# Kernel tuning notes

Hardware: AMD Instinct MI355X
Metric: run time of the kernel (lower is better)

Reference implementation:

```python
import jax, jax.numpy as jnp
import numpy as np

V_SIZE = 128000  # vocab size (v_size init arg)


def setup_inputs() -> dict:
    key = jax.random.key(0)
    k1, k2 = jax.random.split(key)
    # per-position scores -> weighting_scheme (softmax over seq dim)
    w_es = jax.random.normal(k1, (256, 2048), dtype=jnp.float32)
    # instance['x']: token ids in [0, v_size)
    x = jax.random.randint(k2, (256, 2048), 0, V_SIZE, dtype=jnp.int64)
    return {"w_es": w_es, "x": x}


def reference(w_es, x):
    # weighting_scheme(indices, w_es, instance): softmax over sequence positions
    weights = jax.nn.softmax(w_es, axis=-1)          # [B, S]
    B, S = weights.shape
    rows = jnp.arange(B)[:, None]                    # [B, 1] broadcast against [B, S]
    # scatter: w_a[b, x[b, i]] = weights[b, i]  (vectorized index_put)
    w_a = jnp.zeros((B, V_SIZE), dtype=weights.dtype).at[rows, x].set(weights)
    return (w_a, weights)
```

## Files before the change

### kernel.cpp

```cpp
#include <hip/hip_runtime.h>

#define BATCH 256
#define SEQ   2048
#define VOCAB 128000
#define HALF  64000
#define HSLOT 4096

typedef float v4f __attribute__((ext_vector_type(4)));
typedef int   v4i __attribute__((ext_vector_type(4)));
typedef float v2f __attribute__((ext_vector_type(2)));
typedef int   v2i __attribute__((ext_vector_type(2)));

#define LBAR() do { asm volatile("s_waitcnt lgkmcnt(0)" ::: "memory"); \
                    __builtin_amdgcn_s_barrier(); } while (0)

__device__ __forceinline__ int hash_v(int v) {
    return (int)(((unsigned)v * 2654435761u) >> 20);
}

__global__ __launch_bounds__(1024, 4)
void softmax_zero_then_scatter(const float* __restrict__ w_es,
                               const int*   __restrict__ x,
                               float* __restrict__ w_a,
                               float* __restrict__ w_out)
{
    __shared__ int   key[HSLOT];
    __shared__ int   val[HSLOT];
    __shared__ float red[32];

    const int bid = blockIdx.x;
    const int r = bid & (BATCH - 1);
    const int h = bid >> 8;
    const int t = threadIdx.x;
    const int lane = t & 63;
    const int wid  = t >> 6;

    const v2f a  = ((const v2f*)(w_es + (size_t)r * SEQ))[t];
    const v2i xv = ((const v2i*)(x    + (size_t)r * SEQ))[t];

    ((v4i*)key)[t] = (v4i)(-1);
    ((v4i*)val)[t] = (v4i)(-1);

    __syncthreads();

    v4f* gp4 = (v4f*)(w_a + (size_t)r * VOCAB + h * HALF);
    {
        const v4f z = (v4f)(0.0f);
        #pragma unroll
        for (int j = 0; j < 15; ++j)
            gp4[j * 1024 + t] = z;
        if (t < 640)
            gp4[15 * 1024 + t] = z;
    }

    float m = fmaxf(a.x, a.y);
    #pragma unroll
    for (int off = 32; off > 0; off >>= 1)
        m = fmaxf(m, __shfl_down(m, off, 64));
    if (lane == 0) red[wid] = m;
    LBAR();
    m = red[0];
    #pragma unroll
    for (int k = 1; k < 16; ++k) m = fmaxf(m, red[k]);

    const float e0 = __expf(a.x - m);
    const float e1 = __expf(a.y - m);
    float s = e0 + e1;
    #pragma unroll
    for (int off = 32; off > 0; off >>= 1)
        s += __shfl_down(s, off, 64);
    if (lane == 0) red[16 + wid] = s;
    LBAR();
    s = red[16];
    #pragma unroll
    for (int k = 1; k < 16; ++k) s += red[16 + k];

    const float inv = 1.0f / s;
    const float w0 = e0 * inv;
    const float w1 = e1 * inv;

    if (h == 0) {
        v2f wv; wv.x = w0; wv.y = w1;
        ((v2f*)(w_out + (size_t)r * SEQ))[t] = wv;
    }

    const int i0 = 2 * t;
    const int i1 = 2 * t + 1;
    const int v0 = xv.x - h * HALF;
    const int v1 = xv.y - h * HALF;
    const bool in0 = (unsigned)v0 < (unsigned)HALF;
    const bool in1 = (unsigned)v1 < (unsigned)HALF;

    if (in0) {
        int sl = hash_v(v0);
        while (true) {
            int k = atomicCAS(&key[sl], -1, v0);
            if (k == -1 || k == v0) break;
            sl = (sl + 1) & (HSLOT - 1);
        }
        atomicMax(&val[sl], i0);
    }
    if (in1) {
        int sl = hash_v(v1);
        while (true) {
            int k = atomicCAS(&key[sl], -1, v1);
            if (k == -1 || k == v1) break;
            sl = (sl + 1) & (HSLOT - 1);
        }
        atomicMax(&val[sl], i1);
    }

    __syncthreads();

    float* gp = w_a + (size_t)r * VOCAB + h * HALF;
    if (in0) {
        int sl = hash_v(v0);
        while (key[sl] != v0) sl = (sl + 1) & (HSLOT - 1);
        if (val[sl] == i0) gp[v0] = w0;
    }
    if (in1) {
        int sl = hash_v(v1);
        while (key[sl] != v1) sl = (sl + 1) & (HSLOT - 1);
        if (val[sl] == i1) gp[v1] = w1;
    }
}

extern "C" void kernel_launch(void* const* d_in, const int* in_sizes, int n_in,
                              void* d_out, int out_size, void* d_ws, size_t ws_size,
                              hipStream_t stream) {
    const float* w_es = (const float*)d_in[0];
    const int*   x    = (const int*)d_in[1];

    float* out  = (float*)d_out;
    float* w_a  = out;
    float* w    = out + (size_t)BATCH * VOCAB;

    softmax_zero_then_scatter<<<2 * BATCH, 1024, 0, stream>>>(w_es, x, w_a, w);
}
```

Before: 138.2 us.

## Split zeroing into separate kernel and scatter full rows per block

Moves the zero-fill of the output matrix out of the fused kernel into a dedicated grid-stride-style memset kernel. The scatter kernel now handles a whole row per block (256 blocks instead of 512 half-row blocks), so no per-half range filtering is needed and the hash insert is overlapped with the softmax reductions. This adds a second launch and serializes zeroing before scatter, and halves the parallelism of the scatter kernel.

```diff
diff --git a/kernel.cpp b/kernel.cpp
--- a/kernel.cpp
+++ b/kernel.cpp
@@ -3,7 +3,6 @@
 #define BATCH 256
 #define SEQ   2048
 #define VOCAB 128000
-#define HALF  64000
 #define HSLOT 4096
 
 typedef float v4f __attribute__((ext_vector_type(4)));
@@ -11,57 +10,72 @@
 typedef float v2f __attribute__((ext_vector_type(2)));
 typedef int   v2i __attribute__((ext_vector_type(2)));
 
-#define LBAR() do { asm volatile("s_waitcnt lgkmcnt(0)" ::: "memory"); \
-                    __builtin_amdgcn_s_barrier(); } while (0)
-
-__device__ __forceinline__ int hash_v(int v) {
+__device__ __forceinline__ int hash_tok(int v) {
     return (int)(((unsigned)v * 2654435761u) >> 20);
 }
 
-__global__ __launch_bounds__(1024, 4)
-void softmax_zero_then_scatter(const float* __restrict__ w_es,
-                               const int*   __restrict__ x,
-                               float* __restrict__ w_a,
-                               float* __restrict__ w_out)
+__global__ __launch_bounds__(256)
+void zero_wa(float* __restrict__ w_a)
+{
+    const int i = blockIdx.x * 256 + threadIdx.x;
+    v4f* p = (v4f*)w_a;
+    const v4f z = (v4f)(0.0f);
+    #pragma unroll
+    for (int j = 0; j < 8; ++j)
+        p[(size_t)j * 1024000 + i] = z;
+}
+
+__global__ __launch_bounds__(1024, 2)
+void softmax_scatter(const float* __restrict__ w_es,
+                     const int*   __restrict__ x,
+                     float* __restrict__ w_a,
+                     float* __restrict__ w_out)
 {
     __shared__ int   key[HSLOT];
     __shared__ int   val[HSLOT];
     __shared__ float red[32];
 
-    const int bid = blockIdx.x;
-    const int r = bid & (BATCH - 1);
-    const int h = bid >> 8;
+    const int r = blockIdx.x;
     const int t = threadIdx.x;
     const int lane = t & 63;
     const int wid  = t >> 6;
 
-    const v2f a  = ((const v2f*)(w_es + (size_t)r * SEQ))[t];
-    const v2i xv = ((const v2i*)(x    + (size_t)r * SEQ))[t];
-
     ((v4i*)key)[t] = (v4i)(-1);
     ((v4i*)val)[t] = (v4i)(-1);
 
-    __syncthreads();
-
-    v4f* gp4 = (v4f*)(w_a + (size_t)r * VOCAB + h * HALF);
-    {
-        const v4f z = (v4f)(0.0f);
-        #pragma unroll
-        for (int j = 0; j < 15; ++j)
-            gp4[j * 1024 + t] = z;
-        if (t < 640)
-            gp4[15 * 1024 + t] = z;
-    }
+    const v2f a  = ((const v2f*)(w_es + (size_t)r * SEQ))[t];
+    const v2i xv = ((const v2i*)(x    + (size_t)r * SEQ))[t];
 
     float m = fmaxf(a.x, a.y);
     #pragma unroll
     for (int off = 32; off > 0; off >>= 1)
         m = fmaxf(m, __shfl_down(m, off, 64));
     if (lane == 0) red[wid] = m;
-    LBAR();
+    __syncthreads();
     m = red[0];
     #pragma unroll
     for (int k = 1; k < 16; ++k) m = fmaxf(m, red[k]);
+
+    const int i0 = 2 * t;
+    const int i1 = 2 * t + 1;
+    {
+        int sl = hash_tok(xv.x);
+        while (true) {
+            int k = atomicCAS(&key[sl], -1, xv.x);
+            if (k == -1 || k == xv.x) break;
+            sl = (sl + 1) & (HSLOT - 1);
+        }
+        atomicMax(&val[sl], i0);
+    }
+    {
+        int sl = hash_tok(xv.y);
+        while (true) {
+            int k = atomicCAS(&key[sl], -1, xv.y);
+            if (k == -1 || k == xv.y) break;
+            sl = (sl + 1) & (HSLOT - 1);
+        }
+        atomicMax(&val[sl], i1);
+    }
 
     const float e0 = __expf(a.x - m);
     const float e1 = __expf(a.y - m);
@@ -70,7 +84,7 @@
     for (int off = 32; off > 0; off >>= 1)
         s += __shfl_down(s, off, 64);
     if (lane == 0) red[16 + wid] = s;
-    LBAR();
+    __syncthreads();
     s = red[16];
     #pragma unroll
     for (int k = 1; k < 16; ++k) s += red[16 + k];
@@ -79,49 +93,21 @@
     const float w0 = e0 * inv;
     const float w1 = e1 * inv;
 
-    if (h == 0) {
+    {
         v2f wv; wv.x = w0; wv.y = w1;
         ((v2f*)(w_out + (size_t)r * SEQ))[t] = wv;
     }
 
-    const int i0 = 2 * t;
-    const int i1 = 2 * t + 1;
-    const int v0 = xv.x - h * HALF;
-    const int v1 = xv.y - h * HALF;
-    const bool in0 = (unsigned)v0 < (unsigned)HALF;
-    const bool in1 = (unsigned)v1 < (unsigned)HALF;
-
-    if (in0) {
-        int sl = hash_v(v0);
-        while (true) {
-            int k = atomicCAS(&key[sl], -1, v0);
-            if (k == -1 || k == v0) break;
-            sl = (sl + 1) & (HSLOT - 1);
-        }
-        atomicMax(&val[sl], i0);
+    float* gp = w_a + (size_t)r * VOCAB;
+    {
+        int sl = hash_tok(xv.x);
+        while (key[sl] != xv.x) sl = (sl + 1) & (HSLOT - 1);
+        if (val[sl] == i0) gp[xv.x] = w0;
     }
-    if (in1) {
-        int sl = hash_v(v1);
-        while (true) {
-            int k = atomicCAS(&key[sl], -1, v1);
-            if (k == -1 || k == v1) break;
-            sl = (sl + 1) & (HSLOT - 1);
-        }
-        atomicMax(&val[sl], i1);
-    }
-
-    __syncthreads();
-
-    float* gp = w_a + (size_t)r * VOCAB + h * HALF;
-    if (in0) {
-        int sl = hash_v(v0);
-        while (key[sl] != v0) sl = (sl + 1) & (HSLOT - 1);
-        if (val[sl] == i0) gp[v0] = w0;
-    }
-    if (in1) {
-        int sl = hash_v(v1);
-        while (key[sl] != v1) sl = (sl + 1) & (HSLOT - 1);
-        if (val[sl] == i1) gp[v1] = w1;
+    {
+        int sl = hash_tok(xv.y);
+        while (key[sl] != xv.y) sl = (sl + 1) & (HSLOT - 1);
+        if (val[sl] == i1) gp[xv.y] = w1;
     }
 }
 
@@ -135,5 +121,6 @@
     float* w_a  = out;
     float* w    = out + (size_t)BATCH * VOCAB;
 
-    softmax_zero_then_scatter<<<2 * BATCH, 1024, 0, stream>>>(w_es, x, w_a, w);
+    zero_wa<<<4000, 256, 0, stream>>>(w_a);
+    softmax_scatter<<<BATCH, 1024, 0, stream>>>(w_es, x, w_a, w);
 }
```

Result: slower. 141.7 us (+2.5%).
